# Kernel tuning notes

Measured on AMD Instinct MI355X. Metric: run time of the kernel, lower is better.

The kernel has to match this reference:

```python
import jax, jax.numpy as jnp
import numpy as np

N_QUBITS = 12
N_LAYERS = 4
BATCH = 1024


def _ry(theta):
    # Batched RY(theta): (...,) -> (..., 2, 2) complex64
    c = jnp.cos(theta / 2)
    s = jnp.sin(theta / 2)
    m = jnp.stack([jnp.stack([c, -s], -1), jnp.stack([s, c], -1)], -2)
    return m.astype(jnp.complex64)


def _rot(phi, theta, omega):
    # PennyLane Rot(phi, theta, omega) = RZ(omega) @ RY(theta) @ RZ(phi)
    c = jnp.cos(theta / 2)
    s = jnp.sin(theta / 2)
    ep = jnp.exp(-0.5j * (phi + omega))  # e^{-i(phi+omega)/2}
    em = jnp.exp(0.5j * (phi - omega))   # e^{ i(phi-omega)/2}
    m00 = ep * c
    m01 = -em * s
    m10 = jnp.conj(em) * s
    m11 = jnp.conj(ep) * c
    m = jnp.stack([jnp.stack([m00, m01], -1), jnp.stack([m10, m11], -1)], -2)
    return m.astype(jnp.complex64)


def _apply_1q(state, U, wire, n):
    # state: (B, 2^n); U: (2,2) or batched (B,2,2). Wire 0 = most significant bit.
    B = state.shape[0]
    st = state.reshape(B, 2 ** wire, 2, 2 ** (n - 1 - wire))
    if U.ndim == 2:
        st = jnp.einsum('ij,bajc->baic', U, st)
    else:
        st = jnp.einsum('bij,bajc->baic', U, st)
    return st.reshape(B, 2 ** n)


def _cnot(state, c, t, n):
    # CNOT(control=c, target=t): flip target bit where control bit == 1.
    B = state.shape[0]
    lo, hi = (c, t) if c < t else (t, c)
    st = state.reshape(B, 2 ** lo, 2, 2 ** (hi - lo - 1), 2, 2 ** (n - 1 - hi))
    c_ax = 2 if c < t else 4
    t_ax = 6 - c_ax
    s0 = jax.lax.index_in_dim(st, 0, c_ax, keepdims=True)
    s1 = jax.lax.index_in_dim(st, 1, c_ax, keepdims=True)
    s1 = jnp.flip(s1, axis=t_ax)
    st = jnp.concatenate([s0, s1], axis=c_ax)
    return st.reshape(B, 2 ** n)


def _circuit(x, weights):
    # AngleEmbedding(rotation='Y') + StronglyEntanglingLayers + per-wire PauliZ expvals
    B, n = x.shape
    state = jnp.zeros((B, 2 ** n), jnp.complex64).at[:, 0].set(1.0)
    for w in range(n):  # angle embedding: RY(x[:, w]) on wire w (batched gate)
        state = _apply_1q(state, _ry(x[:, w]), w, n)
    n_layers = weights.shape[0]
    for l in range(n_layers):
        for w in range(n):
            state = _apply_1q(state, _rot(weights[l, w, 0], weights[l, w, 1], weights[l, w, 2]), w, n)
        r = (l % (n - 1)) + 1  # default StronglyEntanglingLayers range
        for w in range(n):
            state = _cnot(state, w, (w + r) % n, n)
    probs = jnp.real(state * jnp.conj(state))  # (B, 2^n)
    zs = []
    for w in range(n):
        p = probs.reshape(B, 2 ** w, 2, 2 ** (n - 1 - w))
        zs.append((p[:, :, 0, :] - p[:, :, 1, :]).sum((1, 2)))
    return jnp.stack(zs, -1)  # (B, n) PauliZ expectation values


def setup_inputs() -> dict:
    key = jax.random.key(0)
    k1, k2, k3 = jax.random.split(key, 3)
    x = jax.random.uniform(k1, (BATCH, N_QUBITS), jnp.float32, -jnp.pi, jnp.pi)
    weights = jax.random.uniform(k2, (N_LAYERS, N_QUBITS, 3), jnp.float32, 0.0, 2 * jnp.pi)
    head_w = jax.random.normal(k3, (1, N_QUBITS), jnp.float32) * 0.1
    head_b = jnp.zeros((1,), jnp.float32)
    return {"x": x, "weights": weights, "head_w": head_w, "head_b": head_b}


def reference(x, weights, head_w, head_b):
    z = _circuit(x, weights)              # (B, n_qubits), values in [-1, 1]
    y = z @ head_w.T + head_b             # (B, 1)
    return y[:, 0]                        # squeeze(-1)
```

## Files before the change

kernel.cpp:

```cpp
#include <hip/hip_runtime.h>

#define NQ 12
#define NSTATES 4096
#define NLAYERS 4
#define NGATES 48
#define NGROUPS 12
#define TPB 256

struct Sched { unsigned m[NGATES]; unsigned sel[NGATES]; unsigned zrow[NQ]; };

constexpr Sched make_sched() {
    Sched s{};
    unsigned rows[NQ] = {}, bcols[NQ] = {};
    for (int b = 0; b < NQ; ++b) { rows[b] = 1u << b; bcols[b] = 1u << b; }
    int g = 0;
    for (int w = 0; w < NQ; ++w) { int b = NQ - 1 - w; s.m[g] = bcols[b]; s.sel[g] = rows[b]; ++g; }
    for (int l = 0; l < NLAYERS; ++l) {
        if (l > 0)
            for (int w = 0; w < NQ; ++w) { int b = NQ - 1 - w; s.m[g] = bcols[b]; s.sel[g] = rows[b]; ++g; }
        int r = (l % (NQ - 1)) + 1;
        for (int w = 0; w < NQ; ++w) {
            int c = w, t = (w + r) % NQ;
            int bc = NQ - 1 - c, bt = NQ - 1 - t;
            rows[bt] ^= rows[bc];
            bcols[bc] ^= bcols[bt];
        }
    }
    for (int w = 0; w < NQ; ++w) s.zrow[w] = rows[NQ - 1 - w];
    return s;
}

constexpr unsigned swz(unsigned j) { return j ^ (((j >> 4) ^ (j >> 8)) & 0xFu); }

struct Group {
    unsigned sel[4];
    unsigned swzc[16];
    unsigned cparbits[4];
    int npos[8];
};
struct Plan {
    Group g[NGROUPS];
    unsigned zrow[NQ];
    unsigned zparbits[NQ];
};

constexpr bool inv4(const unsigned m[4], int p0, int p1, int p2, int p3) {
    int pv[4] = {p0, p1, p2, p3};
    unsigned rows[4] = {};
    for (int i = 0; i < 4; ++i) {
        unsigned r = 0;
        for (int k = 0; k < 4; ++k) r |= ((m[i] >> pv[k]) & 1u) << k;
        rows[i] = r;
    }
    unsigned used = 0; int rank = 0;
    for (int c = 0; c < 4; ++c) {
        int pr = -1;
        for (int r = 0; r < 4; ++r)
            if (!((used >> r) & 1u) && ((rows[r] >> c) & 1u)) { pr = r; break; }
        if (pr < 0) continue;
        used |= 1u << pr; ++rank;
        for (int r = 0; r < 4; ++r)
            if (r != pr && ((rows[r] >> c) & 1u)) rows[r] ^= rows[pr];
    }
    return rank == 4;
}

constexpr int popc12(unsigned v) { int c = 0; for (int i = 0; i < 12; ++i) c += (v >> i) & 1; return c; }
constexpr int msb12(unsigned v) { int m = -1; for (int i = 0; i < 12; ++i) if ((v >> i) & 1) m = i; return m; }

constexpr int coverage(const int piv[4]) {
    bool isp[12] = {};
    for (int i = 0; i < 4; ++i) isp[piv[i]] = true;
    bool seen[4] = {}; int cov = 0, cnt = 0;
    for (int p = 0; p < 12 && cnt < 6; ++p)
        if (!isp[p]) { if (!seen[p & 3]) { seen[p & 3] = true; ++cov; } ++cnt; }
    return cov;
}

constexpr Plan make_plan() {
    Sched s = make_sched();
    Plan pl{};
    for (int w = 0; w < NQ; ++w) pl.zrow[w] = s.zrow[w];
    for (int gi = 0; gi < NGROUPS; ++gi) {
        Group &G = pl.g[gi];
        unsigned m[4] = {};
        for (int i = 0; i < 4; ++i) { m[i] = s.m[gi * 4 + i]; G.sel[i] = s.sel[gi * 4 + i]; }
        int piv[4] = {};
        unsigned bas[4] = {};
        for (int i = 0; i < 4; ++i) {
            unsigned v = m[i];
            for (int k = 0; k < i; ++k) if ((v >> piv[k]) & 1u) v ^= bas[k];
            piv[i] = msb12(v);
            bas[i] = v;
        }
        if (coverage(piv) < 4) {
            int best[4] = {piv[0], piv[1], piv[2], piv[3]};
            int bestcov = coverage(piv);
            for (int a = 0; a < 4 && bestcov < 4; ++a) {
                for (int q = 0; q < 12 && bestcov < 4; ++q) {
                    bool dup = false;
                    for (int i = 0; i < 4; ++i) if (piv[i] == q) dup = true;
                    if (dup) continue;
                    int cand[4] = {piv[0], piv[1], piv[2], piv[3]};
                    cand[a] = q;
                    if (!inv4(m, cand[0], cand[1], cand[2], cand[3])) continue;
                    int cv = coverage(cand);
                    if (cv > bestcov) { bestcov = cv; for (int i = 0; i < 4; ++i) best[i] = cand[i]; }
                }
            }
            for (int i = 0; i < 4; ++i) piv[i] = best[i];
        }
        {
            bool isp[12] = {};
            for (int i = 0; i < 4; ++i) isp[piv[i]] = true;
            int k = 0;
            for (int p = 0; p < 12; ++p) if (!isp[p]) G.npos[k++] = p;
        }
        for (int e = 0; e < 16; ++e) {
            unsigned c = 0;
            for (int q = 0; q < 4; ++q) if ((e >> q) & 1) c ^= m[q];
            G.swzc[e] = swz(c);
        }
        for (int i = 0; i < 4; ++i) {
            unsigned bits = 0;
            for (int e = 0; e < 16; ++e) {
                unsigned c = 0;
                for (int q = 0; q < 4; ++q) if ((e >> q) & 1) c ^= m[q];
                if (popc12(c & G.sel[i]) & 1) bits |= 1u << e;
            }
            G.cparbits[i] = bits;
        }
        if (gi == NGROUPS - 1) {
            for (int w = 0; w < NQ; ++w) {
                unsigned bits = 0;
                for (int e = 0; e < 16; ++e) {
                    unsigned c = 0;
                    for (int q = 0; q < 4; ++q) if ((e >> q) & 1) c ^= m[q];
                    if (popc12(c & s.zrow[w]) & 1) bits |= 1u << e;
                }
                pl.zparbits[w] = bits;
            }
        }
    }
    return pl;
}

__device__ constexpr Plan PLAN = make_plan();

__device__ __forceinline__ float xorf(float a, unsigned s) {
    return __uint_as_float(__float_as_uint(a) ^ s);
}

template <int GI>
__device__ __forceinline__ void do_pass(int tid, float (&ar)[16], float (&ai)[16],
                                        unsigned &jr_out, float2* st, const float4* gmat)
{
    constexpr Group G = PLAN.g[GI];

    unsigned jr = 0;
    #pragma unroll
    for (int k = 0; k < 8; ++k) jr |= ((unsigned)(tid >> k) & 1u) << G.npos[k];
    const unsigned basev = jr ^ (((jr >> 4) ^ (jr >> 8)) & 0xFu);

    if constexpr (GI == 0) {
        #pragma unroll
        for (int e = 0; e < 16; ++e) { ar[e] = 0.0f; ai[e] = 0.0f; }
        if (jr == 0u) ar[0] = 1.0f;
    } else {
        #pragma unroll
        for (int e = 0; e < 16; ++e) {
            float2 v = st[basev ^ G.swzc[e]];
            ar[e] = v.x; ai[e] = v.y;
        }
    }

    #pragma unroll
    for (int i = 0; i < 4; ++i) {
        const float4 uv = gmat[GI * 4 + i];
        const unsigned sgP = (unsigned)(__popc(jr & G.sel[i]) & 1) << 31;
        const float ur = uv.x, vi = uv.w;
        const float ui_p = xorf(uv.y, sgP), ui_n = xorf(uv.y, sgP ^ 0x80000000u);
        const float vr_p = xorf(uv.z, sgP), vr_n = xorf(uv.z, sgP ^ 0x80000000u);
        #pragma unroll
        for (int e = 0; e < 16; ++e) {
            if (e & (1 << i)) continue;
            const int f = e | (1 << i);
            const bool neg = ((G.cparbits[i] >> e) & 1u) != 0;
            const float ui = neg ? ui_n : ui_p;
            const float vr = neg ? vr_n : vr_p;
            const float xr_ = ar[e], xi_ = ai[e];
            const float yr_ = ar[f], yi_ = ai[f];
            ar[e] = fmaf(ur, xr_, fmaf(-ui, xi_, fmaf(vr, yr_, -vi * yi_)));
            ai[e] = fmaf(ur, xi_, fmaf( ui, xr_, fmaf(vr, yi_,  vi * yr_)));
            ar[f] = fmaf(ur, yr_, fmaf( ui, yi_, fmaf(-vr, xr_, -vi * xi_)));
            ai[f] = fmaf(ur, yi_, fmaf(-ui, yr_, fmaf(-vr, xi_,  vi * xr_)));
        }
    }

    if constexpr (GI < NGROUPS - 1) {
        #pragma unroll
        for (int e = 0; e < 16; ++e)
            st[basev ^ G.swzc[e]] = make_float2(ar[e], ai[e]);
        __syncthreads();
    }
    jr_out = jr;
}

template <int GI>
__device__ __forceinline__ void run_from(int tid, float (&ar)[16], float (&ai)[16],
                                         unsigned &jr, float2* st, const float4* gmat)
{
    do_pass<GI>(tid, ar, ai, jr, st, gmat);
    if constexpr (GI + 1 < NGROUPS) run_from<GI + 1>(tid, ar, ai, jr, st, gmat);
}

__global__ __launch_bounds__(TPB)
__attribute__((amdgpu_waves_per_eu(4, 4)))
void qreg_kernel(
    const float* __restrict__ x,
    const float* __restrict__ W,
    const float* __restrict__ hw,
    const float* __restrict__ hb,
    float* __restrict__ out)
{
    __shared__ float2 st[NSTATES];
    __shared__ float4 gmat[NGATES];
    __shared__ float red[TPB / 64];

    const int tid = threadIdx.x;
    const int b = blockIdx.x;

    if (tid < NGATES) {
        const int l = tid / NQ;
        const int w = tid % NQ;
        const float* wp = W + tid * 3;
        float phi = wp[0], th = wp[1], om = wp[2];
        float sn, cs;  sincosf(0.5f * th, &sn, &cs);
        float sa, ca;  sincosf(0.5f * (phi + om), &sa, &ca);
        float sb, cb;  sincosf(0.5f * (phi - om), &sb, &cb);
        float u2r = ca * cs, u2i = -sa * cs;
        float v2r = -cb * sn, v2i = -sb * sn;
        float ur, ui, vr, vi;
        if (l == 0) {
            float s1, c1; sincosf(0.5f * x[b * NQ + w], &s1, &c1);
            ur = u2r * c1 + v2r * s1;  ui = u2i * c1 + v2i * s1;
            vr = v2r * c1 - u2r * s1;  vi = v2i * c1 - u2i * s1;
        } else {
            ur = u2r; ui = u2i; vr = v2r; vi = v2i;
        }
        gmat[tid] = make_float4(ur, ui, vr, vi);
    }
    __syncthreads();

    float ar[16], ai[16];
    unsigned jr = 0;
    run_from<0>(tid, ar, ai, jr, st, gmat);

    float hws[NQ];
    #pragma unroll
    for (int w = 0; w < NQ; ++w) {
        const unsigned sg = (unsigned)(__popc(jr & PLAN.zrow[w]) & 1) << 31;
        hws[w] = xorf(hw[w], sg);
    }
    float acc = 0.0f;
    #pragma unroll
    for (int e = 0; e < 16; ++e) {
        const float prob = fmaf(ar[e], ar[e], ai[e] * ai[e]);
        float coef = 0.0f;
        #pragma unroll
        for (int w = 0; w < NQ; ++w)
            coef += ((PLAN.zparbits[w] >> e) & 1u) ? -hws[w] : hws[w];
        acc = fmaf(prob, coef, acc);
    }

    #pragma unroll
    for (int o = 32; o > 0; o >>= 1) acc += __shfl_xor(acc, o, 64);
    if ((tid & 63) == 0) red[tid >> 6] = acc;
    __syncthreads();
    if (tid == 0) out[b] = red[0] + red[1] + red[2] + red[3] + hb[0];
}

extern "C" void kernel_launch(void* const* d_in, const int* in_sizes, int n_in,
                              void* d_out, int out_size, void* d_ws, size_t ws_size,
                              hipStream_t stream) {
    const float* x  = (const float*)d_in[0];
    const float* W  = (const float*)d_in[1];
    const float* hw = (const float*)d_in[2];
    const float* hb = (const float*)d_in[3];
    float* out = (float*)d_out;

    int B = in_sizes[0] / NQ;
    qreg_kernel<<<B, TPB, 0, stream>>>(x, W, hw, hb, out);
}
```

Measured before the change: 92.51 us.

## Build initial product state analytically, skipping first layer's gate passes

The first 12 gates act on the |0> state with no entanglers between them, so they form a product state. Each thread now computes its 16 amplitudes directly as a tensor product of the per-wire first columns and writes them to shared memory. This removes three of the twelve gate-group passes along with their shared-memory round trips and barriers. The first gate of each remaining pass is also interleaved with the split loads so arithmetic overlaps LDS latency. The cost is an extra barrier and a more intricate schedule layout that must stay consistent with the gate offsets.

```diff
diff --git a/kernel.cpp b/kernel.cpp
--- a/kernel.cpp
+++ b/kernel.cpp
@@ -4,7 +4,8 @@
 #define NSTATES 4096
 #define NLAYERS 4
 #define NGATES 48
-#define NGROUPS 12
+#define NMERGED 12
+#define NGROUPS 9
 #define TPB 256
 
 struct Sched { unsigned m[NGATES]; unsigned sel[NGATES]; unsigned zrow[NQ]; };
@@ -84,7 +85,10 @@
     for (int gi = 0; gi < NGROUPS; ++gi) {
         Group &G = pl.g[gi];
         unsigned m[4] = {};
-        for (int i = 0; i < 4; ++i) { m[i] = s.m[gi * 4 + i]; G.sel[i] = s.sel[gi * 4 + i]; }
+        for (int i = 0; i < 4; ++i) {
+            m[i] = s.m[NMERGED + gi * 4 + i];
+            G.sel[i] = s.sel[NMERGED + gi * 4 + i];
+        }
         int piv[4] = {};
         unsigned bas[4] = {};
         for (int i = 0; i < 4; ++i) {
@@ -162,21 +166,54 @@
     for (int k = 0; k < 8; ++k) jr |= ((unsigned)(tid >> k) & 1u) << G.npos[k];
     const unsigned basev = jr ^ (((jr >> 4) ^ (jr >> 8)) & 0xFu);
 
-    if constexpr (GI == 0) {
-        #pragma unroll
-        for (int e = 0; e < 16; ++e) { ar[e] = 0.0f; ai[e] = 0.0f; }
-        if (jr == 0u) ar[0] = 1.0f;
-    } else {
-        #pragma unroll
-        for (int e = 0; e < 16; ++e) {
+    #pragma unroll
+    for (int e = 0; e < 8; ++e) {
+        float2 v = st[basev ^ G.swzc[e]];
+        ar[e] = v.x; ai[e] = v.y;
+    }
+
+    {
+        const float4 uv = gmat[NMERGED + GI * 4 + 0];
+        const unsigned sgP = (unsigned)(__popc(jr & G.sel[0]) & 1) << 31;
+        const float ur = uv.x, vi = uv.w;
+        const float ui_p = xorf(uv.y, sgP), ui_n = xorf(uv.y, sgP ^ 0x80000000u);
+        const float vr_p = xorf(uv.z, sgP), vr_n = xorf(uv.z, sgP ^ 0x80000000u);
+        #pragma unroll
+        for (int e = 0; e < 8; e += 2) {
+            const int f = e | 1;
+            const bool neg = ((G.cparbits[0] >> e) & 1u) != 0;
+            const float ui = neg ? ui_n : ui_p;
+            const float vr = neg ? vr_n : vr_p;
+            const float xr_ = ar[e], xi_ = ai[e];
+            const float yr_ = ar[f], yi_ = ai[f];
+            ar[e] = fmaf(ur, xr_, fmaf(-ui, xi_, fmaf(vr, yr_, -vi * yi_)));
+            ai[e] = fmaf(ur, xi_, fmaf( ui, xr_, fmaf(vr, yi_,  vi * yr_)));
+            ar[f] = fmaf(ur, yr_, fmaf( ui, yi_, fmaf(-vr, xr_, -vi * xi_)));
+            ai[f] = fmaf(ur, yi_, fmaf(-ui, yr_, fmaf(-vr, xi_,  vi * xr_)));
+        }
+        #pragma unroll
+        for (int e = 8; e < 16; ++e) {
             float2 v = st[basev ^ G.swzc[e]];
             ar[e] = v.x; ai[e] = v.y;
         }
-    }
-
-    #pragma unroll
-    for (int i = 0; i < 4; ++i) {
-        const float4 uv = gmat[GI * 4 + i];
+        #pragma unroll
+        for (int e = 8; e < 16; e += 2) {
+            const int f = e | 1;
+            const bool neg = ((G.cparbits[0] >> e) & 1u) != 0;
+            const float ui = neg ? ui_n : ui_p;
+            const float vr = neg ? vr_n : vr_p;
+            const float xr_ = ar[e], xi_ = ai[e];
+            const float yr_ = ar[f], yi_ = ai[f];
+            ar[e] = fmaf(ur, xr_, fmaf(-ui, xi_, fmaf(vr, yr_, -vi * yi_)));
+            ai[e] = fmaf(ur, xi_, fmaf( ui, xr_, fmaf(vr, yi_,  vi * yr_)));
+            ar[f] = fmaf(ur, yr_, fmaf( ui, yi_, fmaf(-vr, xr_, -vi * xi_)));
+            ai[f] = fmaf(ur, yi_, fmaf(-ui, yr_, fmaf(-vr, xi_,  vi * xr_)));
+        }
+    }
+
+    #pragma unroll
+    for (int i = 1; i < 4; ++i) {
+        const float4 uv = gmat[NMERGED + GI * 4 + i];
         const unsigned sgP = (unsigned)(__popc(jr & G.sel[i]) & 1) << 31;
         const float ur = uv.x, vi = uv.w;
         const float ui_p = xorf(uv.y, sgP), ui_n = xorf(uv.y, sgP ^ 0x80000000u);
@@ -253,6 +290,61 @@
     __syncthreads();
 
     float ar[16], ai[16];
+
+    {
+        float pr = 1.0f, pi = 0.0f;
+        #pragma unroll
+        for (int k = 7; k >= 0; --k) {
+            const float4 g = gmat[7 - k];
+            const bool bset = ((tid >> k) & 1) != 0;
+            const float fr = bset ? -g.z : g.x;
+            const float fi = bset ?  g.w : g.y;
+            const float nr = fmaf(pr, fr, -pi * fi);
+            const float ni = fmaf(pr, fi,  pi * fr);
+            pr = nr; pi = ni;
+        }
+        float t2r[2], t2i[2];
+        {   const float4 g = gmat[8];
+            t2r[0] = fmaf(pr,  g.x, -pi * g.y);  t2i[0] = fmaf(pr, g.y,  pi * g.x);
+            t2r[1] = fmaf(pr, -g.z, -pi * g.w);  t2i[1] = fmaf(pr, g.w, -pi * g.z);
+        }
+        float t4r[4], t4i[4];
+        {   const float4 g = gmat[9];
+            #pragma unroll
+            for (int h = 0; h < 2; ++h) {
+                t4r[2*h]   = fmaf(t2r[h],  g.x, -t2i[h] * g.y);
+                t4i[2*h]   = fmaf(t2r[h],  g.y,  t2i[h] * g.x);
+                t4r[2*h+1] = fmaf(t2r[h], -g.z, -t2i[h] * g.w);
+                t4i[2*h+1] = fmaf(t2r[h],  g.w, -t2i[h] * g.z);
+            }
+        }
+        float t8r[8], t8i[8];
+        {   const float4 g = gmat[10];
+            #pragma unroll
+            for (int h = 0; h < 4; ++h) {
+                t8r[2*h]   = fmaf(t4r[h],  g.x, -t4i[h] * g.y);
+                t8i[2*h]   = fmaf(t4r[h],  g.y,  t4i[h] * g.x);
+                t8r[2*h+1] = fmaf(t4r[h], -g.z, -t4i[h] * g.w);
+                t8i[2*h+1] = fmaf(t4r[h],  g.w, -t4i[h] * g.z);
+            }
+        }
+        {   const float4 g = gmat[11];
+            #pragma unroll
+            for (int h = 0; h < 8; ++h) {
+                ar[2*h]   = fmaf(t8r[h],  g.x, -t8i[h] * g.y);
+                ai[2*h]   = fmaf(t8r[h],  g.y,  t8i[h] * g.x);
+                ar[2*h+1] = fmaf(t8r[h], -g.z, -t8i[h] * g.w);
+                ai[2*h+1] = fmaf(t8r[h],  g.w, -t8i[h] * g.z);
+            }
+        }
+        const unsigned hh = ((unsigned)tid ^ ((unsigned)tid >> 4)) & 0xFu;
+        const unsigned base = (unsigned)tid << 4;
+        #pragma unroll
+        for (int e = 0; e < 16; ++e)
+            st[base | ((unsigned)e ^ hh)] = make_float2(ar[e], ai[e]);
+    }
+    __syncthreads();
+
     unsigned jr = 0;
     run_from<0>(tid, ar, ai, jr, st, gmat);
 
```

After: 88.45 us. -4.4%, faster.

## Build initial product state analytically and switch butterflies to packed float2 math

Applied to the files above, without the earlier changes.

The first layer of 12 single-qubit gates acts on the |0…0> product state, so it is now computed directly as a tensor product per thread instead of through three generic butterfly passes. This cuts the pass count from 12 to 9, removing three rounds of LDS traffic and barriers. Butterflies now use two-wide float vectors so the compiler can emit packed FMA instructions. The second half of the first group's LDS loads is also deferred so it overlaps the first butterflies. The risk is extra register pressure from the temporary product arrays and a changed swizzle for the initial store.

```diff
diff --git a/kernel.cpp b/kernel.cpp
--- a/kernel.cpp
+++ b/kernel.cpp
@@ -1,10 +1,13 @@
 #include <hip/hip_runtime.h>
+
+typedef float v2f __attribute__((ext_vector_type(2)));
 
 #define NQ 12
 #define NSTATES 4096
 #define NLAYERS 4
 #define NGATES 48
-#define NGROUPS 12
+#define NMERGED 12
+#define NGROUPS 9
 #define TPB 256
 
 struct Sched { unsigned m[NGATES]; unsigned sel[NGATES]; unsigned zrow[NQ]; };
@@ -84,7 +87,10 @@
     for (int gi = 0; gi < NGROUPS; ++gi) {
         Group &G = pl.g[gi];
         unsigned m[4] = {};
-        for (int i = 0; i < 4; ++i) { m[i] = s.m[gi * 4 + i]; G.sel[i] = s.sel[gi * 4 + i]; }
+        for (int i = 0; i < 4; ++i) {
+            m[i] = s.m[NMERGED + gi * 4 + i];
+            G.sel[i] = s.sel[NMERGED + gi * 4 + i];
+        }
         int piv[4] = {};
         unsigned bas[4] = {};
         for (int i = 0; i < 4; ++i) {
@@ -151,9 +157,21 @@
     return __uint_as_float(__float_as_uint(a) ^ s);
 }
 
+#define BFLY2(ip, e, f)                                                       \
+    {                                                                         \
+        const bool neg = ((G.cparbits[ip] >> (e)) & 1u) != 0;                 \
+        const float uis = neg ? ui_n : ui_p;                                  \
+        const float vrs = neg ? vr_n : vr_p;                                  \
+        const v2f x = a[e], y = a[f];                                         \
+        const v2f Jx = {-x.y, x.x};                                           \
+        const v2f Jy = {-y.y, y.x};                                           \
+        a[e] = x * ur + Jx * uis + y * vrs + Jy * vi;                         \
+        a[f] = y * ur - Jy * uis - x * vrs + Jx * vi;                         \
+    }
+
 template <int GI>
-__device__ __forceinline__ void do_pass(int tid, float (&ar)[16], float (&ai)[16],
-                                        unsigned &jr_out, float2* st, const float4* gmat)
+__device__ __forceinline__ void do_pass(int tid, v2f (&a)[16],
+                                        unsigned &jr_out, v2f* st, const float4* gmat)
 {
     constexpr Group G = PLAN.g[GI];
 
@@ -162,21 +180,30 @@
     for (int k = 0; k < 8; ++k) jr |= ((unsigned)(tid >> k) & 1u) << G.npos[k];
     const unsigned basev = jr ^ (((jr >> 4) ^ (jr >> 8)) & 0xFu);
 
-    if constexpr (GI == 0) {
-        #pragma unroll
-        for (int e = 0; e < 16; ++e) { ar[e] = 0.0f; ai[e] = 0.0f; }
-        if (jr == 0u) ar[0] = 1.0f;
-    } else {
-        #pragma unroll
-        for (int e = 0; e < 16; ++e) {
-            float2 v = st[basev ^ G.swzc[e]];
-            ar[e] = v.x; ai[e] = v.y;
-        }
-    }
-
-    #pragma unroll
-    for (int i = 0; i < 4; ++i) {
-        const float4 uv = gmat[GI * 4 + i];
+    #pragma unroll
+    for (int e = 0; e < 8; ++e) a[e] = st[basev ^ G.swzc[e]];
+
+    {
+        const float4 uv = gmat[NMERGED + GI * 4 + 0];
+        const unsigned sgP = (unsigned)(__popc(jr & G.sel[0]) & 1) << 31;
+        const float ur = uv.x, vi = uv.w;
+        const float ui_p = xorf(uv.y, sgP), ui_n = xorf(uv.y, sgP ^ 0x80000000u);
+        const float vr_p = xorf(uv.z, sgP), vr_n = xorf(uv.z, sgP ^ 0x80000000u);
+        BFLY2(0, 0, 1)
+        BFLY2(0, 2, 3)
+        BFLY2(0, 4, 5)
+        BFLY2(0, 6, 7)
+        #pragma unroll
+        for (int e = 8; e < 16; ++e) a[e] = st[basev ^ G.swzc[e]];
+        BFLY2(0, 8, 9)
+        BFLY2(0, 10, 11)
+        BFLY2(0, 12, 13)
+        BFLY2(0, 14, 15)
+    }
+
+    #pragma unroll
+    for (int i = 1; i < 4; ++i) {
+        const float4 uv = gmat[NMERGED + GI * 4 + i];
         const unsigned sgP = (unsigned)(__popc(jr & G.sel[i]) & 1) << 31;
         const float ur = uv.x, vi = uv.w;
         const float ui_p = xorf(uv.y, sgP), ui_n = xorf(uv.y, sgP ^ 0x80000000u);
@@ -185,33 +212,25 @@
         for (int e = 0; e < 16; ++e) {
             if (e & (1 << i)) continue;
             const int f = e | (1 << i);
-            const bool neg = ((G.cparbits[i] >> e) & 1u) != 0;
-            const float ui = neg ? ui_n : ui_p;
-            const float vr = neg ? vr_n : vr_p;
-            const float xr_ = ar[e], xi_ = ai[e];
-            const float yr_ = ar[f], yi_ = ai[f];
-            ar[e] = fmaf(ur, xr_, fmaf(-ui, xi_, fmaf(vr, yr_, -vi * yi_)));
-            ai[e] = fmaf(ur, xi_, fmaf( ui, xr_, fmaf(vr, yi_,  vi * yr_)));
-            ar[f] = fmaf(ur, yr_, fmaf( ui, yi_, fmaf(-vr, xr_, -vi * xi_)));
-            ai[f] = fmaf(ur, yi_, fmaf(-ui, yr_, fmaf(-vr, xi_,  vi * xr_)));
+            BFLY2(i, e, f)
         }
     }
 
     if constexpr (GI < NGROUPS - 1) {
         #pragma unroll
         for (int e = 0; e < 16; ++e)
-            st[basev ^ G.swzc[e]] = make_float2(ar[e], ai[e]);
+            st[basev ^ G.swzc[e]] = a[e];
         __syncthreads();
     }
     jr_out = jr;
 }
 
 template <int GI>
-__device__ __forceinline__ void run_from(int tid, float (&ar)[16], float (&ai)[16],
-                                         unsigned &jr, float2* st, const float4* gmat)
+__device__ __forceinline__ void run_from(int tid, v2f (&a)[16],
+                                         unsigned &jr, v2f* st, const float4* gmat)
 {
-    do_pass<GI>(tid, ar, ai, jr, st, gmat);
-    if constexpr (GI + 1 < NGROUPS) run_from<GI + 1>(tid, ar, ai, jr, st, gmat);
+    do_pass<GI>(tid, a, jr, st, gmat);
+    if constexpr (GI + 1 < NGROUPS) run_from<GI + 1>(tid, a, jr, st, gmat);
 }
 
 __global__ __launch_bounds__(TPB)
@@ -223,7 +242,7 @@
     const float* __restrict__ hb,
     float* __restrict__ out)
 {
-    __shared__ float2 st[NSTATES];
+    __shared__ v2f st[NSTATES];
     __shared__ float4 gmat[NGATES];
     __shared__ float red[TPB / 64];
 
@@ -252,9 +271,59 @@
     }
     __syncthreads();
 
-    float ar[16], ai[16];
+    v2f a[16];
+
+    {
+        v2f p = {1.0f, 0.0f};
+        #pragma unroll
+        for (int k = 7; k >= 0; --k) {
+            const float4 g = gmat[7 - k];
+            const bool bset = ((tid >> k) & 1) != 0;
+            const float fr = bset ? -g.z : g.x;
+            const float fi = bset ?  g.w : g.y;
+            const v2f Jp = {-p.y, p.x};
+            p = p * fr + Jp * fi;
+        }
+        v2f t2[2], t4[4], t8[8];
+        {   const float4 g = gmat[8];
+            const v2f Jp = {-p.y, p.x};
+            t2[0] = p * g.x + Jp * g.y;
+            t2[1] = p * (-g.z) + Jp * g.w;
+        }
+        {   const float4 g = gmat[9];
+            #pragma unroll
+            for (int h = 0; h < 2; ++h) {
+                const v2f Jt = {-t2[h].y, t2[h].x};
+                t4[2*h]   = t2[h] * g.x + Jt * g.y;
+                t4[2*h+1] = t2[h] * (-g.z) + Jt * g.w;
+            }
+        }
+        {   const float4 g = gmat[10];
+            #pragma unroll
+            for (int h = 0; h < 4; ++h) {
+                const v2f Jt = {-t4[h].y, t4[h].x};
+                t8[2*h]   = t4[h] * g.x + Jt * g.y;
+                t8[2*h+1] = t4[h] * (-g.z) + Jt * g.w;
+            }
+        }
+        {   const float4 g = gmat[11];
+            #pragma unroll
+            for (int h = 0; h < 8; ++h) {
+                const v2f Jt = {-t8[h].y, t8[h].x};
+                a[2*h]   = t8[h] * g.x + Jt * g.y;
+                a[2*h+1] = t8[h] * (-g.z) + Jt * g.w;
+            }
+        }
+        const unsigned hh = ((unsigned)tid ^ ((unsigned)tid >> 4)) & 0xFu;
+        const unsigned base = (unsigned)tid << 4;
+        #pragma unroll
+        for (int e = 0; e < 16; ++e)
+            st[base | ((unsigned)e ^ hh)] = a[e];
+    }
+    __syncthreads();
+
     unsigned jr = 0;
-    run_from<0>(tid, ar, ai, jr, st, gmat);
+    run_from<0>(tid, a, jr, st, gmat);
 
     float hws[NQ];
     #pragma unroll
@@ -265,7 +334,7 @@
     float acc = 0.0f;
     #pragma unroll
     for (int e = 0; e < 16; ++e) {
-        const float prob = fmaf(ar[e], ar[e], ai[e] * ai[e]);
+        const float prob = fmaf(a[e].x, a[e].x, a[e].y * a[e].y);
         float coef = 0.0f;
         #pragma unroll
         for (int w = 0; w < NQ; ++w)
```

Measured after the change: 92.07 us. No clear change (-0.5%).
